# Performance work log

Measured on AMD Instinct MI355X. Metric: run time of the kernel, lower is better.

The kernel has to match this reference:

```python
import jax, jax.numpy as jnp
import numpy as np

TWO_PI = 2.0 * np.pi

# ---- batched real statevector simulator (RY + CNOT circuits are real) ----

def _ry(state, theta, w, n):
    # state: (B, 2**n); theta scalar or (B,)
    half = theta * 0.5
    c, s = jnp.cos(half), jnp.sin(half)
    if jnp.ndim(theta):
        c = c[:, None, None]
        s = s[:, None, None]
    st = state.reshape(-1, 2 ** w, 2, 2 ** (n - w - 1))
    a, b = st[:, :, 0], st[:, :, 1]
    out = jnp.stack([c * a - s * b, s * a + c * b], axis=2)
    return out.reshape(-1, 2 ** n)


def _cnot(state, c, t, n):
    st = state.reshape((-1,) + (2,) * n)
    ax_c, ax_t = c + 1, t + 1
    s0 = jnp.take(st, 0, axis=ax_c)
    s1 = jnp.take(st, 1, axis=ax_c)
    ax_t2 = ax_t - 1 if ax_t > ax_c else ax_t
    s1 = jnp.flip(s1, axis=ax_t2)  # X on target in control=1 block
    out = jnp.stack([s0, s1], axis=ax_c)
    return out.reshape(-1, 2 ** n)


def _expz(state, w, n):
    st = state.reshape(-1, 2 ** w, 2, 2 ** (n - w - 1))
    p = jnp.sum(st * st, axis=(1, 3))  # (B, 2)
    return p[:, 0] - p[:, 1]


def _product_state(angles):
    # RY(angle_i)|0> per wire -> product state; angles: (B, n)
    half = angles * 0.5
    c, s = jnp.cos(half), jnp.sin(half)
    B, n = angles.shape
    state = jnp.ones((B, 1), angles.dtype)
    for i in range(n):
        v = jnp.stack([c[:, i], s[:, i]], axis=-1)  # (B, 2)
        state = (state[:, :, None] * v[:, None, :]).reshape(B, -1)
    return state


EDGE_OPS = [("ry", 0, 0), ("ry", 1, 1), ("cx", 0, 1),
            ("ry", 2, 2), ("ry", 3, 3), ("cx", 3, 2),
            ("ry", 4, 4), ("ry", 5, 5), ("cx", 5, 4),
            ("ry", 6, 6), ("ry", 7, 7), ("cx", 6, 7),
            ("ry", 8, 8), ("ry", 9, 9), ("cx", 8, 9),
            ("ry", 10, 1), ("ry", 11, 2), ("cx", 1, 2),
            ("ry", 12, 7), ("ry", 13, 9), ("cx", 9, 7),
            ("ry", 14, 2), ("ry", 15, 4), ("cx", 2, 4),
            ("ry", 16, 4), ("ry", 17, 7), ("cx", 4, 7),
            ("ry", 18, 7)]

NODE_OPS = [("ry", 0, 0), ("ry", 1, 1), ("cx", 0, 1),
            ("ry", 2, 2), ("ry", 3, 3), ("cx", 3, 2),
            ("ry", 4, 4), ("ry", 5, 5), ("cx", 4, 5),
            ("ry", 6, 6), ("ry", 7, 7), ("cx", 7, 6),
            ("ry", 8, 8), ("ry", 9, 9), ("cx", 8, 9),
            ("ry", 10, 10), ("ry", 11, 11), ("cx", 11, 10),
            ("ry", 12, 12), ("ry", 13, 13), ("cx", 8, 9),
            ("ry", 14, 14),
            ("ry", 15, 1), ("ry", 16, 2), ("cx", 1, 2),
            ("ry", 14, 5), ("ry", 15, 6), ("cx", 6, 5),
            ("ry", 16, 9), ("ry", 17, 10), ("cx", 9, 10),
            ("ry", 18, 13), ("ry", 19, 14), ("cx", 9, 10),
            ("ry", 19, 2), ("ry", 20, 5), ("cx", 2, 5),
            ("ry", 21, 10), ("ry", 22, 13), ("cx", 13, 10),
            ("ry", 23, 5), ("ry", 24, 10),
            ("ry", 25, 0), ("ry", 26, 5), ("cx", 0, 5),
            ("ry", 27, 10), ("ry", 28, 14), ("cx", 14, 10),
            ("ry", 29, 5), ("ry", 30, 10)]


def _run(state, ops, theta, n):
    for op in ops:
        if op[0] == "ry":
            state = _ry(state, theta[op[1]], op[2], n)
        else:
            state = _cnot(state, op[1], op[2], n)
    return state


@jax.checkpoint
def _edge_circ(feats, theta):  # feats: (E, 10) -> (E,)
    state = _product_state(feats)
    state = _run(state, EDGE_OPS, theta, 10)
    return _expz(state, 7, 10)


@jax.checkpoint
def _node_circ(feats, theta):  # feats: (N, 15) -> (N, 2)
    state = _product_state(feats)
    state = _run(state, NODE_OPS, theta, 15)
    return jnp.stack([_expz(state, 5, 15), _expz(state, 10, 15)], axis=1)


def _edge_net(H, Ri, Ro, theta_edge):
    bo = Ro.T @ H  # (E, 5)
    bi = Ri.T @ H  # (E, 5)
    B = jnp.concatenate([bo, bi], axis=1)  # (E, 10)
    z = _edge_circ(B, theta_edge)
    return (1.0 - z) / 2.0  # (E,)


def _node_net(H, e, Ri, Ro, theta_node):
    bo = Ro.T @ H
    bi = Ri.T @ H
    Rwo = Ro * e  # (N, E) weighted by edge scores
    Rwi = Ri * e
    mi = Rwi @ bo  # (N, 5)
    mo = Rwo @ bi  # (N, 5)
    M = jnp.concatenate([mi, mo, H], axis=1)  # (N, 15)
    z = _node_circ(M, theta_node)  # (N, 2)
    return TWO_PI * (1.0 - z) / 2.0


N_ITERS = 2


def _gnn(X, Ri, Ro, W, theta_edge, theta_node):
    H = jax.nn.sigmoid(X @ W) * TWO_PI  # (N, 2)
    H = jnp.concatenate([H, X], axis=1)  # (N, 5)
    e = _edge_net(H, Ri, Ro, theta_edge)
    for _ in range(N_ITERS):
        Hn = _node_net(H, e, Ri, Ro, theta_node)
        H = jnp.concatenate([Hn, X], axis=1)
        e = _edge_net(H, Ri, Ro, theta_edge)
    return e


def setup_inputs() -> dict:
    N, E = 384, 1280
    key = jax.random.key(0)
    k1, k2, k3, k4, k5, k6 = jax.random.split(key, 6)
    X = jax.random.uniform(k1, (N, 3), dtype=jnp.float32)
    snd = jax.random.randint(k2, (E,), 0, N)
    rcv = jax.random.randint(k3, (E,), 0, N)
    Ro = jax.nn.one_hot(snd, N, dtype=jnp.float32).T  # (N, E)
    Ri = jax.nn.one_hot(rcv, N, dtype=jnp.float32).T  # (N, E)
    W = jax.random.normal(k4, (3, 2), dtype=jnp.float32)
    theta_edge = jax.random.uniform(k5, (19,), dtype=jnp.float32, maxval=TWO_PI)
    theta_node = jax.random.uniform(k6, (31,), dtype=jnp.float32, maxval=TWO_PI)
    return {"X": X, "Ri": Ri, "Ro": Ro, "W": W,
            "theta_edge": theta_edge, "theta_node": theta_node}


def reference(X, Ri, Ro, W, theta_edge, theta_node):
    return _gnn(X, Ri, Ro, W, theta_edge, theta_node)
```

## Files before the change

### kernel.cpp

```cpp
#include <hip/hip_runtime.h>
#include <math.h>

#define N_NODES 384
#define N_EDGES 1280

template <int M>
__device__ __forceinline__ float lxor_f(float x)
{
    if constexpr (M == 1) {
        return __builtin_bit_cast(float, __builtin_amdgcn_mov_dpp(
            __builtin_bit_cast(int, x), 0xB1, 0xF, 0xF, true));
    } else if constexpr (M == 2) {
        return __builtin_bit_cast(float, __builtin_amdgcn_mov_dpp(
            __builtin_bit_cast(int, x), 0x4E, 0xF, 0xF, true));
    } else if constexpr (M == 8) {
        return __builtin_bit_cast(float, __builtin_amdgcn_mov_dpp(
            __builtin_bit_cast(int, x), 0x128, 0xF, 0xF, true));
    } else {
        return __shfl_xor(x, M, 64);
    }
}

template <int K, int M>
__device__ __forceinline__ void ryr2(float2 (&a)[K], float c_, float s_)
{
#pragma unroll
    for (int k = 0; k < K; k++)
        if ((k & M) == 0) {
            float2 u = a[k], v = a[k | M];
            a[k].x     = c_ * u.x - s_ * v.x;
            a[k].y     = c_ * u.y - s_ * v.y;
            a[k | M].x = s_ * u.x + c_ * v.x;
            a[k | M].y = s_ * u.y + c_ * v.y;
        }
}

template <int K>
__device__ __forceinline__ void ryc2(float2 (&a)[K], float c_, float s_)
{
#pragma unroll
    for (int k = 0; k < K; k++) {
        float x = a[k].x, y = a[k].y;
        a[k].x = c_ * x - s_ * y;
        a[k].y = s_ * x + c_ * y;
    }
}

template <int K, int LM>
__device__ __forceinline__ void ryl2(float2 (&a)[K], int lane, float c_, float s_)
{
    const float ss = (lane & LM) ? s_ : -s_;
#pragma unroll
    for (int k = 0; k < K; k++) {
        float ox = lxor_f<LM>(a[k].x);
        float oy = lxor_f<LM>(a[k].y);
        a[k].x = fmaf(ss, ox, c_ * a[k].x);
        a[k].y = fmaf(ss, oy, c_ * a[k].y);
    }
}

template <int K, int TM>
__device__ __forceinline__ void cxl2(float2 (&a)[K], bool ctrl)
{
#pragma unroll
    for (int k = 0; k < K; k++) {
        float ox = lxor_f<TM>(a[k].x);
        float oy = lxor_f<TM>(a[k].y);
        a[k].x = ctrl ? ox : a[k].x;
        a[k].y = ctrl ? oy : a[k].y;
    }
}

template <int K, int TM>
__device__ __forceinline__ void cxr2(float2 (&a)[K], bool ctrl)
{
#pragma unroll
    for (int k = 0; k < K; k++)
        if ((k & TM) == 0) {
            float2 u = a[k], v = a[k | TM];
            a[k].x      = ctrl ? v.x : u.x;
            a[k].y      = ctrl ? v.y : u.y;
            a[k | TM].x = ctrl ? u.x : v.x;
            a[k | TM].y = ctrl ? u.y : v.y;
        }
}

template <int K>
__device__ __forceinline__ void cxc2(float2 (&a)[K], bool ctrl)
{
#pragma unroll
    for (int k = 0; k < K; k++) {
        float x = a[k].x, y = a[k].y;
        a[k].x = ctrl ? y : x;
        a[k].y = ctrl ? x : y;
    }
}

template <int K, int CM, int TM>
__device__ __forceinline__ void cxrr2(float2 (&a)[K])
{
#pragma unroll
    for (int k = 0; k < K; k++)
        if ((k & CM) && !(k & TM)) {
            float2 t = a[k]; a[k] = a[k | TM]; a[k | TM] = t;
        }
}

template <int K, int TM>
__device__ __forceinline__ void cxcr2(float2 (&a)[K])
{
#pragma unroll
    for (int k = 0; k < K; k++)
        if ((k & TM) == 0) {
            float t = a[k].y; a[k].y = a[k | TM].y; a[k | TM].y = t;
        }
}

__global__ __launch_bounds__(256) void prep_kernel(
    const float* __restrict__ X, const float* __restrict__ Ri,
    const float* __restrict__ Ro, const float* __restrict__ W,
    const float* __restrict__ th_e, const float* __restrict__ th_n,
    int* __restrict__ snd, int* __restrict__ rcv, float* __restrict__ H0,
    float* __restrict__ cte, float* __restrict__ ste,
    float* __restrict__ ctn, float* __restrict__ stn,
    float* __restrict__ M)
{
    int idx = blockIdx.x * blockDim.x + threadIdx.x;
    if (idx < N_NODES * N_EDGES) {
        int n = idx / N_EDGES, e = idx - n * N_EDGES;
        if (Ro[idx] > 0.5f) snd[e] = n;
        if (Ri[idx] > 0.5f) rcv[e] = n;
    }
    if (idx < N_NODES) {
        int n = idx;
        float x0 = X[n * 3 + 0], x1 = X[n * 3 + 1], x2 = X[n * 3 + 2];
        float t0 = x0 * W[0] + x1 * W[2] + x2 * W[4];
        float t1 = x0 * W[1] + x1 * W[3] + x2 * W[5];
        const float TP = 6.2831853071795864769f;
        H0[n * 5 + 0] = TP / (1.f + __expf(-t0));
        H0[n * 5 + 1] = TP / (1.f + __expf(-t1));
        H0[n * 5 + 2] = x0;
        H0[n * 5 + 3] = x1;
        H0[n * 5 + 4] = x2;
    } else if (idx >= 512 && idx < 512 + 19) {
        int j = idx - 512;
        float h = 0.5f * th_e[j];
        cte[j] = __cosf(h); ste[j] = __sinf(h);
    } else if (idx >= 576 && idx < 576 + 31) {
        int j = idx - 576;
        float h = 0.5f * th_n[j];
        ctn[j] = __cosf(h); stn[j] = __sinf(h);
    } else if (idx >= 1024 && idx < 1024 + N_NODES * 10) {
        M[idx - 1024] = 0.f;
    }
}

__global__ __launch_bounds__(256) void edge_kernel(
    const float* __restrict__ H, const int* __restrict__ snd, const int* __restrict__ rcv,
    const float* __restrict__ cte, const float* __restrict__ ste,
    const float* __restrict__ th_e,
    float* __restrict__ out, float* __restrict__ M, int do_agg)
{
    const int e = blockIdx.x * 4 + (threadIdx.x >> 6);
    const int lane = threadIdx.x & 63;
    const int se = snd[e], re = rcv[e];

    float f[10];
#pragma unroll
    for (int k = 0; k < 5; k++) { f[k] = H[se * 5 + k]; f[5 + k] = H[re * 5 + k]; }

    float cw[10], sw[10];
#pragma unroll
    for (int w = 0; w < 10; w++) {
        float h = 0.5f * (f[w] + th_e[w]);
        sw[w] = __sinf(h);
        cw[w] = __cosf(h);
    }

    float pl = 1.f;
    pl *= (lane & 1)  ? sw[1] : cw[1];
    pl *= (lane & 2)  ? sw[0] : cw[0];
    pl *= (lane & 4)  ? sw[3] : cw[3];
    pl *= (lane & 8)  ? sw[5] : cw[5];
    pl *= (lane & 16) ? sw[6] : cw[6];
    pl *= (lane & 32) ? sw[8] : cw[8];
    float2 a[8];
#pragma unroll
    for (int k = 0; k < 8; k++) {
        float p = pl;
        p *= (k & 1) ? sw[7] : cw[7];
        p *= (k & 2) ? sw[2] : cw[2];
        p *= (k & 4) ? sw[4] : cw[4];
        a[k].x = p * cw[9];
        a[k].y = p * sw[9];
    }

    cxl2<8, 1>(a, (lane & 2) != 0);
    cxr2<8, 2>(a, (lane & 4) != 0);
    cxr2<8, 4>(a, (lane & 8) != 0);
    cxr2<8, 1>(a, (lane & 16) != 0);
    cxc2<8>(a, (lane & 32) != 0);
    ryl2<8, 1>(a, lane, cte[10], ste[10]);
    ryr2<8, 2>(a, cte[11], ste[11]);
    cxr2<8, 2>(a, (lane & 1) != 0);
    ryr2<8, 1>(a, cte[12], ste[12]);
    ryc2<8>(a, cte[13], ste[13]);
    cxcr2<8, 1>(a);
    ryr2<8, 2>(a, cte[14], ste[14]);
    ryr2<8, 4>(a, cte[15], ste[15]);
    cxrr2<8, 2, 4>(a);
    ryr2<8, 4>(a, cte[16], ste[16]);
    ryr2<8, 1>(a, cte[17], ste[17]);
    cxrr2<8, 4, 1>(a);
    ryr2<8, 1>(a, cte[18], ste[18]);

    float z = 0.f;
#pragma unroll
    for (int k = 0; k < 8; k++) {
        float v = a[k].x * a[k].x + a[k].y * a[k].y;
        z += (k & 1) ? -v : v;
    }
#pragma unroll
    for (int o = 32; o > 0; o >>= 1) z += __shfl_xor(z, o, 64);
    float ev = 0.5f * (1.f - z);

    if (lane == 0) out[e] = ev;
    if (do_agg) {
        if (lane < 5)       atomicAdd(&M[re * 10 + lane], ev * f[lane]);
        else if (lane < 10) atomicAdd(&M[se * 10 + lane], ev * f[lane]);
    }
}

__global__ __launch_bounds__(64) void node_kernel(
    const float* __restrict__ H, float* __restrict__ M,
    const float* __restrict__ ctn, const float* __restrict__ stn,
    const float* __restrict__ th_n,
    const float* __restrict__ X, float* __restrict__ Hout)
{
    const int n = blockIdx.x;
    const int tid = threadIdx.x;
    const int lane = tid;

    __shared__ float cw[12], sw[12];

    if (tid < 12) {
        const int wire_of_pb[12] = {10, 5, 2, 13, 3, 14, 7, 1, 0, 6, 4, 11};
        int w_ = wire_of_pb[tid];
        float ang = ((w_ < 10) ? M[n * 10 + w_] : H[n * 5 + (w_ - 10)]) + th_n[w_];
        float h = 0.5f * ang;
        sw[tid] = __sinf(h);
        cw[tid] = __cosf(h);
    }
    __syncthreads();
    if (tid < 10) M[n * 10 + tid] = 0.f;

    float h1721 = 0.5f * (th_n[17] + th_n[21]);
    float h1822 = 0.5f * (th_n[18] + th_n[22]);
    float h1928 = 0.5f * (th_n[19] + th_n[28]);
    float h2326 = 0.5f * (th_n[23] + th_n[26]);
    float h2427 = 0.5f * (th_n[24] + th_n[27]);
    float ms1721 = __sinf(h1721), mc1721 = __cosf(h1721);
    float ms1822 = __sinf(h1822), mc1822 = __cosf(h1822);
    float ms1928 = __sinf(h1928), mc1928 = __cosf(h1928);
    float ms2326 = __sinf(h2326), mc2326 = __cosf(h2326);
    float ms2427 = __sinf(h2427), mc2427 = __cosf(h2427);

    float pw = 1.f;
    pw *= (lane & 1)  ? sw[6]  : cw[6];
    pw *= (lane & 2)  ? sw[7]  : cw[7];
    pw *= (lane & 4)  ? sw[8]  : cw[8];
    pw *= (lane & 8)  ? sw[9]  : cw[9];
    pw *= (lane & 16) ? sw[10] : cw[10];
    pw *= (lane & 32) ? sw[11] : cw[11];
    float2 a[32];
#pragma unroll
    for (int k = 0; k < 32; k++) {
        float p = pw;
        p *= (k & 1)  ? sw[0] : cw[0];
        p *= (k & 2)  ? sw[1] : cw[1];
        p *= (k & 4)  ? sw[2] : cw[2];
        p *= (k & 8)  ? sw[3] : cw[3];
        p *= (k & 16) ? sw[4] : cw[4];
        a[k].x = p * cw[5];
        a[k].y = p * sw[5];
    }

    cxl2<32, 2>(a, (lane & 4) != 0);
    cxrr2<32, 16, 4>(a);
    cxr2<32, 2>(a, (lane & 16) != 0);
    cxl2<32, 8>(a, (lane & 1) != 0);
    cxr2<32, 1>(a, (lane & 32) != 0);
    ryl2<32, 2>(a, lane, ctn[15], stn[15]);
    ryr2<32, 4>(a, ctn[16], stn[16]);
    cxr2<32, 4>(a, (lane & 2) != 0);
    ryr2<32, 2>(a, ctn[14], stn[14]);
    ryl2<32, 8>(a, lane, ctn[15], stn[15]);
    cxr2<32, 2>(a, (lane & 8) != 0);
    ryr2<32, 1>(a, mc1721, ms1721);
    ryr2<32, 8>(a, mc1822, ms1822);
    ryc2<32>(a, mc1928, ms1928);
    ryr2<32, 4>(a, ctn[19], stn[19]);
    ryr2<32, 2>(a, ctn[20], stn[20]);
    cxrr2<32, 4, 2>(a);
    cxrr2<32, 8, 1>(a);
    ryr2<32, 2>(a, mc2326, ms2326);
    ryr2<32, 1>(a, mc2427, ms2427);
    ryl2<32, 4>(a, lane, ctn[25], stn[25]);
    cxr2<32, 2>(a, (lane & 4) != 0);
    cxcr2<32, 1>(a);
    ryr2<32, 2>(a, ctn[29], stn[29]);
    ryr2<32, 1>(a, ctn[30], stn[30]);

    float z5 = 0.f, z10 = 0.f;
#pragma unroll
    for (int k = 0; k < 32; k++) {
        float v = a[k].x * a[k].x + a[k].y * a[k].y;
        z5  += (k & 2) ? -v : v;
        z10 += (k & 1) ? -v : v;
    }
#pragma unroll
    for (int o = 32; o > 0; o >>= 1) {
        z5  += __shfl_xor(z5, o, 64);
        z10 += __shfl_xor(z10, o, 64);
    }
    if (lane == 0) {
        const float PI_ = 3.14159265358979323846f;
        Hout[n * 5 + 0] = PI_ * (1.f - z5);
        Hout[n * 5 + 1] = PI_ * (1.f - z10);
        Hout[n * 5 + 2] = X[n * 3 + 0];
        Hout[n * 5 + 3] = X[n * 3 + 1];
        Hout[n * 5 + 4] = X[n * 3 + 2];
    }
}

extern "C" void kernel_launch(void* const* d_in, const int* in_sizes, int n_in,
                              void* d_out, int out_size, void* d_ws, size_t ws_size,
                              hipStream_t stream)
{
    const float* X    = (const float*)d_in[0];
    const float* Ri   = (const float*)d_in[1];
    const float* Ro   = (const float*)d_in[2];
    const float* W    = (const float*)d_in[3];
    const float* th_e = (const float*)d_in[4];
    const float* th_n = (const float*)d_in[5];
    float* out = (float*)d_out;

    float* Ha  = (float*)d_ws;
    float* Hb  = Ha + N_NODES * 5;
    float* ev  = Hb + N_NODES * 5;
    int*   snd = (int*)(ev + N_EDGES);
    int*   rcv = snd + N_EDGES;
    float* M   = (float*)(rcv + N_EDGES);
    float* cte = M + N_NODES * 10;
    float* ste = cte + 19;
    float* ctn = ste + 19;
    float* stn = ctn + 31;

    prep_kernel<<<(N_NODES * N_EDGES + 255) / 256, 256, 0, stream>>>(
        X, Ri, Ro, W, th_e, th_n, snd, rcv, Ha, cte, ste, ctn, stn, M);

    edge_kernel<<<N_EDGES / 4, 256, 0, stream>>>(Ha, snd, rcv, cte, ste, th_e, ev, M, 1);
    node_kernel<<<N_NODES, 64, 0, stream>>>(Ha, M, ctn, stn, th_n, X, Hb);

    edge_kernel<<<N_EDGES / 4, 256, 0, stream>>>(Hb, snd, rcv, cte, ste, th_e, ev, M, 1);
    node_kernel<<<N_NODES, 64, 0, stream>>>(Hb, M, ctn, stn, th_n, X, Ha);

    edge_kernel<<<N_EDGES / 4, 256, 0, stream>>>(Ha, snd, rcv, cte, ste, th_e, out, M, 0);
}
```

Before: 38.55 us.

## Fold prep into first edge kernel and replace atomic aggregation with per-node gather

Removes the separate prep kernel. The first edge kernel now finds sender and receiver indices by scanning its column of the one-hot matrices with a wave reduction, computes the initial node features inline, and recomputes gate cosines and sines per wave. Edge kernels write per-edge weighted messages to a buffer instead of issuing atomicAdds. Node kernels gather those messages by scanning all 1280 edges per node and reducing across the wave, which removes atomics and the M zeroing. The trade is one fewer launch and no atomics against a strided column read of Ri/Ro and redundant edge scans per node.

After: 51.17 us. +32.7%, slower.

```diff
diff --git a/kernel.cpp b/kernel.cpp
--- a/kernel.cpp
+++ b/kernel.cpp
@@ -116,59 +116,22 @@
         }
 }
 
-__global__ __launch_bounds__(256) void prep_kernel(
-    const float* __restrict__ X, const float* __restrict__ Ri,
-    const float* __restrict__ Ro, const float* __restrict__ W,
-    const float* __restrict__ th_e, const float* __restrict__ th_n,
-    int* __restrict__ snd, int* __restrict__ rcv, float* __restrict__ H0,
-    float* __restrict__ cte, float* __restrict__ ste,
-    float* __restrict__ ctn, float* __restrict__ stn,
-    float* __restrict__ M)
-{
-    int idx = blockIdx.x * blockDim.x + threadIdx.x;
-    if (idx < N_NODES * N_EDGES) {
-        int n = idx / N_EDGES, e = idx - n * N_EDGES;
-        if (Ro[idx] > 0.5f) snd[e] = n;
-        if (Ri[idx] > 0.5f) rcv[e] = n;
-    }
-    if (idx < N_NODES) {
-        int n = idx;
-        float x0 = X[n * 3 + 0], x1 = X[n * 3 + 1], x2 = X[n * 3 + 2];
-        float t0 = x0 * W[0] + x1 * W[2] + x2 * W[4];
-        float t1 = x0 * W[1] + x1 * W[3] + x2 * W[5];
-        const float TP = 6.2831853071795864769f;
-        H0[n * 5 + 0] = TP / (1.f + __expf(-t0));
-        H0[n * 5 + 1] = TP / (1.f + __expf(-t1));
-        H0[n * 5 + 2] = x0;
-        H0[n * 5 + 3] = x1;
-        H0[n * 5 + 4] = x2;
-    } else if (idx >= 512 && idx < 512 + 19) {
-        int j = idx - 512;
-        float h = 0.5f * th_e[j];
-        cte[j] = __cosf(h); ste[j] = __sinf(h);
-    } else if (idx >= 576 && idx < 576 + 31) {
-        int j = idx - 576;
-        float h = 0.5f * th_n[j];
-        ctn[j] = __cosf(h); stn[j] = __sinf(h);
-    } else if (idx >= 1024 && idx < 1024 + N_NODES * 10) {
-        M[idx - 1024] = 0.f;
-    }
-}
-
-__global__ __launch_bounds__(256) void edge_kernel(
-    const float* __restrict__ H, const int* __restrict__ snd, const int* __restrict__ rcv,
-    const float* __restrict__ cte, const float* __restrict__ ste,
-    const float* __restrict__ th_e,
-    float* __restrict__ out, float* __restrict__ M, int do_agg)
-{
-    const int e = blockIdx.x * 4 + (threadIdx.x >> 6);
-    const int lane = threadIdx.x & 63;
-    const int se = snd[e], re = rcv[e];
-
-    float f[10];
-#pragma unroll
-    for (int k = 0; k < 5; k++) { f[k] = H[se * 5 + k]; f[5 + k] = H[re * 5 + k]; }
-
+__device__ __forceinline__ void h0_of(int n, const float* __restrict__ X,
+                                      const float* __restrict__ W, float (&h)[5])
+{
+    float x0 = X[n * 3 + 0], x1 = X[n * 3 + 1], x2 = X[n * 3 + 2];
+    float t0 = x0 * W[0] + x1 * W[2] + x2 * W[4];
+    float t1 = x0 * W[1] + x1 * W[3] + x2 * W[5];
+    const float TP = 6.2831853071795864769f;
+    h[0] = TP / (1.f + __expf(-t0));
+    h[1] = TP / (1.f + __expf(-t1));
+    h[2] = x0; h[3] = x1; h[4] = x2;
+}
+
+__device__ __forceinline__ float edge_ev(
+    int lane, const float (&f)[10], const float* __restrict__ th_e,
+    const float (&gc)[9], const float (&gs)[9])
+{
     float cw[10], sw[10];
 #pragma unroll
     for (int w = 0; w < 10; w++) {
@@ -200,19 +163,19 @@
     cxr2<8, 4>(a, (lane & 8) != 0);
     cxr2<8, 1>(a, (lane & 16) != 0);
     cxc2<8>(a, (lane & 32) != 0);
-    ryl2<8, 1>(a, lane, cte[10], ste[10]);
-    ryr2<8, 2>(a, cte[11], ste[11]);
+    ryl2<8, 1>(a, lane, gc[0], gs[0]);
+    ryr2<8, 2>(a, gc[1], gs[1]);
     cxr2<8, 2>(a, (lane & 1) != 0);
-    ryr2<8, 1>(a, cte[12], ste[12]);
-    ryc2<8>(a, cte[13], ste[13]);
+    ryr2<8, 1>(a, gc[2], gs[2]);
+    ryc2<8>(a, gc[3], gs[3]);
     cxcr2<8, 1>(a);
-    ryr2<8, 2>(a, cte[14], ste[14]);
-    ryr2<8, 4>(a, cte[15], ste[15]);
+    ryr2<8, 2>(a, gc[4], gs[4]);
+    ryr2<8, 4>(a, gc[5], gs[5]);
     cxrr2<8, 2, 4>(a);
-    ryr2<8, 4>(a, cte[16], ste[16]);
-    ryr2<8, 1>(a, cte[17], ste[17]);
+    ryr2<8, 4>(a, gc[6], gs[6]);
+    ryr2<8, 1>(a, gc[7], gs[7]);
     cxrr2<8, 4, 1>(a);
-    ryr2<8, 1>(a, cte[18], ste[18]);
+    ryr2<8, 1>(a, gc[8], gs[8]);
 
     float z = 0.f;
 #pragma unroll
@@ -222,48 +185,139 @@
     }
 #pragma unroll
     for (int o = 32; o > 0; o >>= 1) z += __shfl_xor(z, o, 64);
-    float ev = 0.5f * (1.f - z);
-
-    if (lane == 0) out[e] = ev;
-    if (do_agg) {
-        if (lane < 5)       atomicAdd(&M[re * 10 + lane], ev * f[lane]);
-        else if (lane < 10) atomicAdd(&M[se * 10 + lane], ev * f[lane]);
-    }
-}
-
-__global__ __launch_bounds__(64) void node_kernel(
-    const float* __restrict__ H, float* __restrict__ M,
-    const float* __restrict__ ctn, const float* __restrict__ stn,
-    const float* __restrict__ th_n,
-    const float* __restrict__ X, float* __restrict__ Hout)
-{
-    const int n = blockIdx.x;
-    const int tid = threadIdx.x;
-    const int lane = tid;
-
-    __shared__ float cw[12], sw[12];
-
-    if (tid < 12) {
-        const int wire_of_pb[12] = {10, 5, 2, 13, 3, 14, 7, 1, 0, 6, 4, 11};
-        int w_ = wire_of_pb[tid];
-        float ang = ((w_ < 10) ? M[n * 10 + w_] : H[n * 5 + (w_ - 10)]) + th_n[w_];
-        float h = 0.5f * ang;
-        sw[tid] = __sinf(h);
-        cw[tid] = __cosf(h);
-    }
-    __syncthreads();
-    if (tid < 10) M[n * 10 + tid] = 0.f;
-
-    float h1721 = 0.5f * (th_n[17] + th_n[21]);
-    float h1822 = 0.5f * (th_n[18] + th_n[22]);
-    float h1928 = 0.5f * (th_n[19] + th_n[28]);
-    float h2326 = 0.5f * (th_n[23] + th_n[26]);
-    float h2427 = 0.5f * (th_n[24] + th_n[27]);
-    float ms1721 = __sinf(h1721), mc1721 = __cosf(h1721);
-    float ms1822 = __sinf(h1822), mc1822 = __cosf(h1822);
-    float ms1928 = __sinf(h1928), mc1928 = __cosf(h1928);
-    float ms2326 = __sinf(h2326), mc2326 = __cosf(h2326);
-    float ms2427 = __sinf(h2427), mc2427 = __cosf(h2427);
+    return 0.5f * (1.f - z);
+}
+
+template <int MODE>
+__global__ __launch_bounds__(256) void edge_kernel(
+    const float* __restrict__ H,
+    const float* __restrict__ X, const float* __restrict__ W,
+    const float* __restrict__ Ri, const float* __restrict__ Ro,
+    int* __restrict__ snd, int* __restrict__ rcv,
+    const float* __restrict__ th_e,
+    float* __restrict__ EW, float* __restrict__ out)
+{
+    const int e = blockIdx.x * 4 + (threadIdx.x >> 6);
+    const int lane = threadIdx.x & 63;
+
+    int se, re;
+    if constexpr (MODE == 0) {
+        int s_ = 0, r_ = 0;
+#pragma unroll
+        for (int k = 0; k < 6; k++) {
+            int n = lane + 64 * k;
+            if (Ro[n * N_EDGES + e] > 0.5f) s_ = n;
+            if (Ri[n * N_EDGES + e] > 0.5f) r_ = n;
+        }
+#pragma unroll
+        for (int o = 32; o > 0; o >>= 1) {
+            s_ = max(s_, __shfl_xor(s_, o, 64));
+            r_ = max(r_, __shfl_xor(r_, o, 64));
+        }
+        se = s_; re = r_;
+        if (lane == 0) { snd[e] = se; rcv[e] = re; }
+    } else {
+        se = snd[e]; re = rcv[e];
+    }
+
+    float f[10];
+    if constexpr (MODE == 0) {
+        float hs[5], hr[5];
+        h0_of(se, X, W, hs);
+        h0_of(re, X, W, hr);
+#pragma unroll
+        for (int k = 0; k < 5; k++) { f[k] = hs[k]; f[5 + k] = hr[k]; }
+    } else {
+#pragma unroll
+        for (int k = 0; k < 5; k++) { f[k] = H[se * 5 + k]; f[5 + k] = H[re * 5 + k]; }
+    }
+
+    float gc[9], gs[9];
+#pragma unroll
+    for (int j = 0; j < 9; j++) {
+        float h = 0.5f * th_e[10 + j];
+        gs[j] = __sinf(h); gc[j] = __cosf(h);
+    }
+
+    float ev = edge_ev(lane, f, th_e, gc, gs);
+
+    if constexpr (MODE == 2) {
+        if (lane == 0) out[e] = ev;
+    } else {
+        if (lane < 10) EW[e * 10 + lane] = ev * f[lane];
+    }
+}
+
+template <int FIRST>
+__global__ __launch_bounds__(256) void node_kernel(
+    const float* __restrict__ H,
+    const float* __restrict__ X, const float* __restrict__ W,
+    const int* __restrict__ snd, const int* __restrict__ rcv,
+    const float* __restrict__ EW,
+    const float* __restrict__ th_n, float* __restrict__ Hout)
+{
+    const int n = blockIdx.x * 4 + (threadIdx.x >> 6);
+    const int lane = threadIdx.x & 63;
+
+    float mi[5] = {0.f, 0.f, 0.f, 0.f, 0.f};
+    float mo[5] = {0.f, 0.f, 0.f, 0.f, 0.f};
+#pragma unroll
+    for (int c = 0; c < N_EDGES / 64; c++) {
+        int e = lane + c * 64;
+        int se = snd[e], re = rcv[e];
+        if (re == n) {
+#pragma unroll
+            for (int k = 0; k < 5; k++) mi[k] += EW[e * 10 + k];
+        }
+        if (se == n) {
+#pragma unroll
+            for (int k = 0; k < 5; k++) mo[k] += EW[e * 10 + 5 + k];
+        }
+    }
+#pragma unroll
+    for (int o = 32; o > 0; o >>= 1) {
+#pragma unroll
+        for (int k = 0; k < 5; k++) {
+            mi[k] += __shfl_xor(mi[k], o, 64);
+            mo[k] += __shfl_xor(mo[k], o, 64);
+        }
+    }
+
+    float hv[5];
+    if constexpr (FIRST) {
+        h0_of(n, X, W, hv);
+    } else {
+#pragma unroll
+        for (int k = 0; k < 5; k++) hv[k] = H[n * 5 + k];
+    }
+
+    float cw[12], sw[12];
+    {
+        const float base[12] = {hv[0], mo[0], mi[2], hv[3], mi[3], hv[4],
+                                mo[2], mi[1], mi[0], mo[1], mi[4], hv[1]};
+        const int thw[12] = {10, 5, 2, 13, 3, 14, 7, 1, 0, 6, 4, 11};
+#pragma unroll
+        for (int pb = 0; pb < 12; pb++) {
+            float h = 0.5f * (base[pb] + th_n[thw[pb]]);
+            sw[pb] = __sinf(h);
+            cw[pb] = __cosf(h);
+        }
+    }
+
+    float h_;
+    h_ = 0.5f * th_n[15];                float gs15 = __sinf(h_), gc15 = __cosf(h_);
+    h_ = 0.5f * th_n[16];                float gs16 = __sinf(h_), gc16 = __cosf(h_);
+    h_ = 0.5f * th_n[14];                float gs14 = __sinf(h_), gc14 = __cosf(h_);
+    h_ = 0.5f * th_n[19];                float gs19 = __sinf(h_), gc19 = __cosf(h_);
+    h_ = 0.5f * th_n[20];                float gs20 = __sinf(h_), gc20 = __cosf(h_);
+    h_ = 0.5f * th_n[25];                float gs25 = __sinf(h_), gc25 = __cosf(h_);
+    h_ = 0.5f * th_n[29];                float gs29 = __sinf(h_), gc29 = __cosf(h_);
+    h_ = 0.5f * th_n[30];                float gs30 = __sinf(h_), gc30 = __cosf(h_);
+    h_ = 0.5f * (th_n[17] + th_n[21]);   float ms1721 = __sinf(h_), mc1721 = __cosf(h_);
+    h_ = 0.5f * (th_n[18] + th_n[22]);   float ms1822 = __sinf(h_), mc1822 = __cosf(h_);
+    h_ = 0.5f * (th_n[19] + th_n[28]);   float ms1928 = __sinf(h_), mc1928 = __cosf(h_);
+    h_ = 0.5f * (th_n[23] + th_n[26]);   float ms2326 = __sinf(h_), mc2326 = __cosf(h_);
+    h_ = 0.5f * (th_n[24] + th_n[27]);   float ms2427 = __sinf(h_), mc2427 = __cosf(h_);
 
     float pw = 1.f;
     pw *= (lane & 1)  ? sw[6]  : cw[6];
@@ -290,26 +344,26 @@
     cxr2<32, 2>(a, (lane & 16) != 0);
     cxl2<32, 8>(a, (lane & 1) != 0);
     cxr2<32, 1>(a, (lane & 32) != 0);
-    ryl2<32, 2>(a, lane, ctn[15], stn[15]);
-    ryr2<32, 4>(a, ctn[16], stn[16]);
+    ryl2<32, 2>(a, lane, gc15, gs15);
+    ryr2<32, 4>(a, gc16, gs16);
     cxr2<32, 4>(a, (lane & 2) != 0);
-    ryr2<32, 2>(a, ctn[14], stn[14]);
-    ryl2<32, 8>(a, lane, ctn[15], stn[15]);
+    ryr2<32, 2>(a, gc14, gs14);
+    ryl2<32, 8>(a, lane, gc15, gs15);
     cxr2<32, 2>(a, (lane & 8) != 0);
     ryr2<32, 1>(a, mc1721, ms1721);
     ryr2<32, 8>(a, mc1822, ms1822);
     ryc2<32>(a, mc1928, ms1928);
-    ryr2<32, 4>(a, ctn[19], stn[19]);
-    ryr2<32, 2>(a, ctn[20], stn[20]);
+    ryr2<32, 4>(a, gc19, gs19);
+    ryr2<32, 2>(a, gc20, gs20);
     cxrr2<32, 4, 2>(a);
     cxrr2<32, 8, 1>(a);
     ryr2<32, 2>(a, mc2326, ms2326);
     ryr2<32, 1>(a, mc2427, ms2427);
-    ryl2<32, 4>(a, lane, ctn[25], stn[25]);
+    ryl2<32, 4>(a, lane, gc25, gs25);
     cxr2<32, 2>(a, (lane & 4) != 0);
     cxcr2<32, 1>(a);
-    ryr2<32, 2>(a, ctn[29], stn[29]);
-    ryr2<32, 1>(a, ctn[30], stn[30]);
+    ryr2<32, 2>(a, gc29, gs29);
+    ryr2<32, 1>(a, gc30, gs30);
 
     float z5 = 0.f, z10 = 0.f;
 #pragma unroll
@@ -345,25 +399,20 @@
     const float* th_n = (const float*)d_in[5];
     float* out = (float*)d_out;
 
-    float* Ha  = (float*)d_ws;
-    float* Hb  = Ha + N_NODES * 5;
-    float* ev  = Hb + N_NODES * 5;
-    int*   snd = (int*)(ev + N_EDGES);
+    int*   snd = (int*)d_ws;
     int*   rcv = snd + N_EDGES;
-    float* M   = (float*)(rcv + N_EDGES);
-    float* cte = M + N_NODES * 10;
-    float* ste = cte + 19;
-    float* ctn = ste + 19;
-    float* stn = ctn + 31;
-
-    prep_kernel<<<(N_NODES * N_EDGES + 255) / 256, 256, 0, stream>>>(
-        X, Ri, Ro, W, th_e, th_n, snd, rcv, Ha, cte, ste, ctn, stn, M);
-
-    edge_kernel<<<N_EDGES / 4, 256, 0, stream>>>(Ha, snd, rcv, cte, ste, th_e, ev, M, 1);
-    node_kernel<<<N_NODES, 64, 0, stream>>>(Ha, M, ctn, stn, th_n, X, Hb);
-
-    edge_kernel<<<N_EDGES / 4, 256, 0, stream>>>(Hb, snd, rcv, cte, ste, th_e, ev, M, 1);
-    node_kernel<<<N_NODES, 64, 0, stream>>>(Hb, M, ctn, stn, th_n, X, Ha);
-
-    edge_kernel<<<N_EDGES / 4, 256, 0, stream>>>(Ha, snd, rcv, cte, ste, th_e, out, M, 0);
-}
+    float* EW  = (float*)(rcv + N_EDGES);
+    float* Hb  = EW + N_EDGES * 10;
+    float* Ha2 = Hb + N_NODES * 5;
+
+    edge_kernel<0><<<N_EDGES / 4, 256, 0, stream>>>(
+        nullptr, X, W, Ri, Ro, snd, rcv, th_e, EW, nullptr);
+    node_kernel<1><<<N_NODES / 4, 256, 0, stream>>>(
+        nullptr, X, W, snd, rcv, EW, th_n, Hb);
+    edge_kernel<1><<<N_EDGES / 4, 256, 0, stream>>>(
+        Hb, X, W, Ri, Ro, snd, rcv, th_e, EW, nullptr);
+    node_kernel<0><<<N_NODES / 4, 256, 0, stream>>>(
+        Hb, X, W, snd, rcv, EW, th_n, Ha2);
+    edge_kernel<2><<<N_EDGES / 4, 256, 0, stream>>>(
+        Ha2, X, W, Ri, Ro, snd, rcv, th_e, nullptr, out);
+}
```
